# Kernel optimization log

Measured on AMD Instinct MI355X. Metric: run time of the kernel, lower is better.

## Reference

```python
import jax, jax.numpy as jnp
import numpy as np

SIGMA_COLOR = 0.1
SIGMA_SPATIAL = 5.0
RADIUS = 8


def setup_inputs() -> dict:
    key = jax.random.key(0)
    images = jax.random.uniform(key, (16, 3, 768, 768), dtype=jnp.float32)
    return {"images": images}


def _spatial_affinity(h, w):
    # coordinates of each cell in the (h, w) feature grid, flattened to N = h*w
    y = jnp.repeat(jnp.arange(h, dtype=jnp.float32), w)  # [N]
    x = jnp.tile(jnp.arange(w, dtype=jnp.float32), h)    # [N]
    y_diff = y[:, None] - y[None, :]                      # [N, N]
    x_diff = x[:, None] - x[None, :]                      # [N, N]
    spatial_dist = y_diff ** 2 + x_diff ** 2
    aff = jnp.exp(-spatial_dist / (2.0 * SIGMA_SPATIAL ** 2))
    mask = (jnp.abs(y_diff) <= RADIUS) & (jnp.abs(x_diff) <= RADIUS)
    return aff * mask.astype(aff.dtype)                   # [N, N]


def reference(images):
    B, C, H, W = images.shape
    h, w = H // 16, W // 16
    N = h * w
    # bilinear resize, half-pixel centers == torch align_corners=False
    img_r = jax.image.resize(images, (B, C, h, w), method="bilinear", antialias=False)
    feats = img_r.reshape(B, C, N).transpose(0, 2, 1)     # [B, N, C]
    # ||f_i - f_j||^2 = |f_i|^2 + |f_j|^2 - 2 f_i . f_j  (avoids [B,N,N,C] diff tensor)
    sq = jnp.sum(feats * feats, axis=-1)                  # [B, N]
    dots = jnp.einsum("bic,bjc->bij", feats, feats)       # [B, N, N]
    color_dist = jnp.maximum(sq[:, :, None] + sq[:, None, :] - 2.0 * dots, 0.0)
    color_aff = jnp.exp(-color_dist / (2.0 * SIGMA_COLOR ** 2))  # [B, N, N]
    spatial_aff = _spatial_affinity(h, w)                 # [N, N]
    return color_aff * spatial_aff[None, :, :]            # [B, N, N]
```

## Files before the change

### kernel.cpp

```cpp
#include <hip/hip_runtime.h>

#define BATCH 16
#define CH    3
#define HIN   768
#define WIN   768
#define HS    48
#define WS    48
#define NPIX  (HS * WS)
#define QPR   (NPIX / 4)

__global__ void downsample_kernel(const float* __restrict__ img,
                                  float4* __restrict__ feats) {
    int idx = blockIdx.x * blockDim.x + threadIdx.x;
    if (idx >= BATCH * NPIX) return;
    int b = idx / NPIX;
    int n = idx - b * NPIX;
    int y = n / WS;
    int x = n - y * WS;
    int iy = 16 * y + 7;
    int ix = 16 * x + 7;
    const float* base = img + (size_t)b * CH * HIN * WIN;
    float f[3];
#pragma unroll
    for (int c = 0; c < 3; ++c) {
        const float* p = base + (size_t)c * HIN * WIN;
        const float* r0 = p + (size_t)iy * WIN + ix;
        const float* r1 = r0 + WIN;
        f[c] = 0.25f * (r0[0] + r0[1] + r1[0] + r1[1]);
    }
    feats[idx] = make_float4(f[0], f[1], f[2], 0.0f);
}

__global__ void affinity_kernel(const float4* __restrict__ feats,
                                float4* __restrict__ out) {
    unsigned int t = blockIdx.x * blockDim.x + threadIdx.x;
    const unsigned int total = (unsigned int)BATCH * NPIX * QPR;
    if (t >= total) return;

    unsigned int q  = t % QPR;
    unsigned int bi = t / QPR;
    unsigned int i  = bi % NPIX;
    unsigned int b  = bi / NPIX;

    int j0  = (int)q * 4;
    int yj  = j0 / WS;
    int xj0 = j0 - yj * WS;
    int yi  = (int)i / WS;
    int xi  = (int)i - yi * WS;

    int dy = yi - yj;
    float4 res;
    if (dy > 8 || dy < -8) {
        res = make_float4(0.f, 0.f, 0.f, 0.f);
    } else {
        const float4* frow = feats + (size_t)b * NPIX;
        float4 fi = frow[i];
        float sdy = (float)(dy * dy);
        float v[4];
#pragma unroll
        for (int k = 0; k < 4; ++k) {
            int dx = xi - (xj0 + k);
            float4 fj = frow[j0 + k];
            float d0 = fi.x - fj.x;
            float d1 = fi.y - fj.y;
            float d2 = fi.z - fj.z;
            float cd = d0 * d0 + d1 * d1 + d2 * d2;
            float sd = sdy + (float)(dx * dx);
            float e  = __expf(-50.0f * cd - 0.02f * sd);
            v[k] = (dx > 8 || dx < -8) ? 0.0f : e;
        }
        res = make_float4(v[0], v[1], v[2], v[3]);
    }
    out[(size_t)t] = res;
}

extern "C" void kernel_launch(void* const* d_in, const int* in_sizes, int n_in,
                              void* d_out, int out_size, void* d_ws, size_t ws_size,
                              hipStream_t stream) {
    const float* img = (const float*)d_in[0];
    float4* feats = (float4*)d_ws;
    float4* out   = (float4*)d_out;

    {
        int threads = BATCH * NPIX;
        int block = 256;
        int grid = (threads + block - 1) / block;
        downsample_kernel<<<grid, block, 0, stream>>>(img, feats);
    }
    {
        unsigned int quads = (unsigned int)BATCH * NPIX * QPR;
        int block = 256;
        unsigned int grid = (quads + block - 1) / block;
        affinity_kernel<<<grid, block, 0, stream>>>(feats, out);
    }
}
```

Before: 383.7 us.

## Zero-fill output then compute only the 17x17 spatial window per row

Replaces the dense per-quad affinity kernel with a grid-stride zero-fill of the whole output, followed by a patch kernel. The patch kernel has one block per (batch,i) row and computes only the 289 entries inside the radius window. This removes index math and exp work for the masked-out entries, leaving the fill as a pure bandwidth-bound store. The cost is an extra kernel launch, plus scattered partial-line writes to memory the fill already wrote.

After: 452.9 us. 1.18x slower.

```diff
diff --git a/kernel.cpp b/kernel.cpp
--- a/kernel.cpp
+++ b/kernel.cpp
@@ -7,7 +7,8 @@
 #define HS    48
 #define WS    48
 #define NPIX  (HS * WS)
-#define QPR   (NPIX / 4)
+#define PSZ   17
+#define QTOT  ((size_t)BATCH * NPIX * (NPIX / 4))
 
 __global__ void downsample_kernel(const float* __restrict__ img,
                                   float4* __restrict__ feats) {
@@ -31,47 +32,43 @@
     feats[idx] = make_float4(f[0], f[1], f[2], 0.0f);
 }
 
-__global__ void affinity_kernel(const float4* __restrict__ feats,
-                                float4* __restrict__ out) {
-    unsigned int t = blockIdx.x * blockDim.x + threadIdx.x;
-    const unsigned int total = (unsigned int)BATCH * NPIX * QPR;
-    if (t >= total) return;
+__global__ __launch_bounds__(256) void fill_zero_kernel(float4* __restrict__ out) {
+    size_t stride = (size_t)gridDim.x * blockDim.x;
+    size_t t = (size_t)blockIdx.x * blockDim.x + threadIdx.x;
+    const float4 z = make_float4(0.f, 0.f, 0.f, 0.f);
+    for (size_t q = t; q < QTOT; q += stride) {
+        out[q] = z;
+    }
+}
 
-    unsigned int q  = t % QPR;
-    unsigned int bi = t / QPR;
-    unsigned int i  = bi % NPIX;
-    unsigned int b  = bi / NPIX;
+__global__ __launch_bounds__(320) void patch_kernel(const float4* __restrict__ feats,
+                                                    float* __restrict__ out) {
+    int bi = blockIdx.x;
+    int i  = bi % NPIX;
+    int b  = bi / NPIX;
+    int yi = i / WS;
+    int xi = i - yi * WS;
+    const float4* frow = feats + (size_t)b * NPIX;
+    float4 fi = frow[i];
 
-    int j0  = (int)q * 4;
-    int yj  = j0 / WS;
-    int xj0 = j0 - yj * WS;
-    int yi  = (int)i / WS;
-    int xi  = (int)i - yi * WS;
-
-    int dy = yi - yj;
-    float4 res;
-    if (dy > 8 || dy < -8) {
-        res = make_float4(0.f, 0.f, 0.f, 0.f);
-    } else {
-        const float4* frow = feats + (size_t)b * NPIX;
-        float4 fi = frow[i];
-        float sdy = (float)(dy * dy);
-        float v[4];
-#pragma unroll
-        for (int k = 0; k < 4; ++k) {
-            int dx = xi - (xj0 + k);
-            float4 fj = frow[j0 + k];
-            float d0 = fi.x - fj.x;
-            float d1 = fi.y - fj.y;
-            float d2 = fi.z - fj.z;
-            float cd = d0 * d0 + d1 * d1 + d2 * d2;
-            float sd = sdy + (float)(dx * dx);
-            float e  = __expf(-50.0f * cd - 0.02f * sd);
-            v[k] = (dx > 8 || dx < -8) ? 0.0f : e;
-        }
-        res = make_float4(v[0], v[1], v[2], v[3]);
+    int e = threadIdx.x;
+    if (e >= PSZ * PSZ) return;
+    int r = e / PSZ;
+    int c = e - r * PSZ;
+    int yj = yi - 8 + r;
+    int xj = xi - 8 + c;
+    if ((unsigned)yj < HS && (unsigned)xj < WS) {
+        int j = yj * WS + xj;
+        float4 fj = frow[j];
+        float d0 = fi.x - fj.x;
+        float d1 = fi.y - fj.y;
+        float d2 = fi.z - fj.z;
+        float cd = d0 * d0 + d1 * d1 + d2 * d2;
+        int dy = 8 - r;
+        int dx = 8 - c;
+        float sd = (float)(dy * dy + dx * dx);
+        out[(size_t)bi * NPIX + j] = __expf(-50.0f * cd - 0.02f * sd);
     }
-    out[(size_t)t] = res;
 }
 
 extern "C" void kernel_launch(void* const* d_in, const int* in_sizes, int n_in,
@@ -79,8 +76,14 @@
                               hipStream_t stream) {
     const float* img = (const float*)d_in[0];
     float4* feats = (float4*)d_ws;
-    float4* out   = (float4*)d_out;
+    float4* out4  = (float4*)d_out;
+    float*  out   = (float*)d_out;
 
+    {
+        int block = 256;
+        int grid  = 2048;
+        fill_zero_kernel<<<grid, block, 0, stream>>>(out4);
+    }
     {
         int threads = BATCH * NPIX;
         int block = 256;
@@ -88,9 +91,8 @@
         downsample_kernel<<<grid, block, 0, stream>>>(img, feats);
     }
     {
-        unsigned int quads = (unsigned int)BATCH * NPIX * QPR;
-        int block = 256;
-        unsigned int grid = (quads + block - 1) / block;
-        affinity_kernel<<<grid, block, 0, stream>>>(feats, out);
+        int grid = BATCH * NPIX;
+        int block = 320;
+        patch_kernel<<<grid, block, 0, stream>>>(feats, out);
     }
 }
```
